# Optimization experiments

Hardware: AMD Instinct MI355X
Metric: run time of the kernel (lower is better)

Reference implementation:

```python
import jax, jax.numpy as jnp
import numpy as np

B, N, D, L, OUT = 4, 256, 256, 128, 256
GAMMA, ETA = 1e-4, 1.0


def _gcn_layer(x, alpha, adj, w_alpha, w_vi, w_vj, bias_h, w_node):
    # x:(B,N,D) alpha:(B,N,N,K) adj:(B,N,N)
    xi = jnp.einsum('bid,dk->bik', x, w_vi)  # project BEFORE broadcast (same math)
    xj = jnp.einsum('bjd,dk->bjk', x, w_vj)
    # bias_h:(D,K) broadcasts against trailing (N,K) dims (requires D==N, as in torch)
    H = jax.nn.relu(xi[:, :, None, :] + xj[:, None, :, :] + alpha + bias_h)  # (B,N,N,K)
    AH = jnp.einsum('bij,bijd->bid', adj, H)
    new_x = jax.nn.relu(jnp.einsum('bid,dk->bik', AH, w_node))
    new_alpha = jax.nn.relu(jnp.einsum('bijd,dk->bijk', H, w_alpha))
    return new_x, new_alpha


def setup_inputs() -> dict:
    key = jax.random.key(0)
    ks = jax.random.split(key, 20)
    inv = lambda fan: 1.0 / np.sqrt(fan)
    x = jax.random.normal(ks[0], (B, N, D), dtype=jnp.float32)
    rel_features = jax.random.normal(ks[1], (B, N, N, 6), dtype=jnp.float32)
    adj = jax.random.uniform(ks[2], (B, N, N), dtype=jnp.float32)
    box_num = jnp.concatenate(
        [jnp.full((1, 1), N, dtype=jnp.int32),
         jax.random.randint(ks[3], (B - 1, 1), N // 2, N + 1, dtype=jnp.int32)], axis=0)
    d = {
        'x': x, 'rel_features': rel_features, 'adj': adj, 'box_num': box_num,
        'W_alpha_t': jax.random.normal(ks[4], (6, D)) * inv(6),
        'b_alpha': jnp.zeros((D,), jnp.float32),
        'W_proj': jax.random.normal(ks[5], (D, L)) * inv(D),
        'b_proj': jnp.zeros((L,), jnp.float32),
        'learn_w': jax.random.uniform(ks[6], (L,)),
    }
    for li, base in ((0, 7), (1, 12)):
        d[f'l{li}_w_alpha'] = jax.random.normal(ks[base + 0], (D, OUT)) * inv(D)
        d[f'l{li}_w_vi'] = jax.random.normal(ks[base + 1], (D, OUT)) * inv(D)
        d[f'l{li}_w_vj'] = jax.random.normal(ks[base + 2], (D, OUT)) * inv(D)
        d[f'l{li}_bias_h'] = jax.random.uniform(ks[base + 3], (D, OUT))
        d[f'l{li}_w_node'] = jax.random.normal(ks[base + 4], (D, OUT)) * inv(D)
    return d


def reference(x, rel_features, adj, box_num, W_alpha_t, b_alpha, W_proj, b_proj, learn_w,
              l0_w_alpha, l0_w_vi, l0_w_vj, l0_bias_h, l0_w_node,
              l1_w_alpha, l1_w_vi, l1_w_vj, l1_bias_h, l1_w_node):
    alpha = jnp.einsum('bijc,cd->bijd', rel_features, W_alpha_t) + b_alpha  # (B,N,N,D)

    # ---- GraphLearningLayer ----
    x_hat = x @ W_proj + b_proj  # (B,N,L)
    valid = jnp.arange(N)[None, :] < box_num  # (B,N)
    pair = valid[:, None, :] & valid[:, :, None]  # (B,N,N)
    mask = jnp.where(pair, 0.0, -1.0)[..., None]  # (~mask)*-1 in torch
    dist = jnp.abs(x_hat[:, :, None, :] - x_hat[:, None, :, :]) + mask  # (B,N,N,L)
    out = jax.nn.leaky_relu(jnp.einsum('bijd,d->bij', dist, learn_w))
    out = out - jnp.max(out, axis=-1, keepdims=True)
    soft_adj = jnp.exp(out) * adj
    soft_adj = soft_adj / jnp.sum(soft_adj, axis=-1, keepdims=True) + 1e-10

    # graph learning loss (training branch)
    diff = x_hat[:, :, None, :] - x_hat[:, None, :, :]
    pair_norm = jnp.sqrt(jnp.sum(diff * diff, axis=-1) + 1e-12)  # (B,N,N)
    bn = box_num.astype(jnp.float32)[:, 0]
    dist_loss = jnp.sum(jnp.exp(soft_adj + ETA * pair_norm), axis=(1, 2)) / (bn * bn)
    f_norm = jnp.sqrt(jnp.sum(soft_adj * soft_adj, axis=(1, 2)))
    gl_loss = dist_loss + GAMMA * f_norm  # (B,)

    # ---- GCN stack ----
    adj2 = adj * soft_adj
    x1, alpha1 = _gcn_layer(x, alpha, adj2, l0_w_alpha, l0_w_vi, l0_w_vj, l0_bias_h, l0_w_node)
    x2, _ = _gcn_layer(x1, alpha1, adj2, l1_w_alpha, l1_w_vi, l1_w_vj, l1_bias_h, l1_w_node)
    return x2, soft_adj, gl_loss
```

## Files before the change

kernel.cpp:

```cpp
#include <hip/hip_runtime.h>
#include <hip/hip_bf16.h>

#define NB 4
#define NN 256
#define ND 256
#define NL 128
#define NK 256
static constexpr float GAMMA_C = 1e-4f;
static constexpr float ETA_C = 1.0f;

typedef unsigned int u32;
typedef __attribute__((ext_vector_type(8))) short bf16x8;
typedef __attribute__((ext_vector_type(4))) float f32x4;

__device__ __forceinline__ u32 rne1(float x) {
    u32 a = __float_as_uint(x);
    return (a + 0x7FFFu + ((a >> 16) & 1u)) >> 16;
}
__device__ __forceinline__ float bf2f(u32 v) { return __uint_as_float(v << 16); }
__device__ __forceinline__ u32 pk2(float lo, float hi) {
    union { __hip_bfloat162 h; u32 u; } cv;
    cv.h = __float22bfloat162_rn(make_float2(lo, hi));
    return cv.u;
}

struct GJob {
    const float* A; const float* W; const float* bias; const float* addm;
    float* C; float* CT; int Kd; int Nc; int relu;
};

__device__ __forceinline__ void gemm64_body(
    const float* __restrict__ A, const float* __restrict__ W,
    const float* __restrict__ bias, const float* __restrict__ addm,
    float* __restrict__ C, float* __restrict__ CT, int Kd, int Nc, int relu_act)
{
    __shared__ __align__(16) float As[16][68];
    __shared__ __align__(16) float Ws[16][64];
    int t = threadIdx.x;
    int r0 = blockIdx.x * 64, c0 = blockIdx.y * 64;
    int ty = t >> 4, tx = t & 15;
    float acc[4][4] = {};
    for (int kc = 0; kc < Kd; kc += 16) {
        __syncthreads();
        #pragma unroll
        for (int q = 0; q < 4; ++q) {
            int f = q * 256 + t;
            int row = f >> 4, kk = f & 15;
            As[kk][row] = A[(r0 + row) * Kd + kc + kk];
        }
        #pragma unroll
        for (int q = 0; q < 4; ++q) {
            int f = q * 256 + t;
            int kk = f >> 6, col = f & 63;
            Ws[kk][col] = W[(kc + kk) * Nc + c0 + col];
        }
        __syncthreads();
        #pragma unroll
        for (int kk = 0; kk < 16; ++kk) {
            float4 av = *(const float4*)&As[kk][ty * 4];
            float4 bv = *(const float4*)&Ws[kk][tx * 4];
            float a[4] = {av.x, av.y, av.z, av.w};
            float b[4] = {bv.x, bv.y, bv.z, bv.w};
            #pragma unroll
            for (int i = 0; i < 4; ++i)
                #pragma unroll
                for (int j = 0; j < 4; ++j)
                    acc[i][j] += a[i] * b[j];
        }
    }
    #pragma unroll
    for (int i = 0; i < 4; ++i) {
        int row = r0 + ty * 4 + i;
        #pragma unroll
        for (int j = 0; j < 4; ++j) {
            int col = c0 + tx * 4 + j;
            float v = acc[i][j];
            if (bias) v += bias[col];
            if (addm) v += addm[(row & 255) * Nc + col];
            if (relu_act) v = fmaxf(v, 0.f);
            C[row * Nc + col] = v;
            if (CT) CT[((row >> 8) * Nc + col) * 256 + (row & 255)] = v;
        }
    }
}

__global__ __launch_bounds__(256) void gemm64(
    const float* __restrict__ A, const float* __restrict__ W,
    const float* __restrict__ bias, const float* __restrict__ addm,
    float* __restrict__ C, int M, int Kd, int Nc, int relu_act)
{
    gemm64_body(A, W, bias, addm, C, nullptr, Kd, Nc, relu_act);
}

__global__ __launch_bounds__(256) void gemm64_multi(GJob j0, GJob j1, GJob j2)
{
    GJob jb = (blockIdx.z == 0) ? j0 : (blockIdx.z == 1) ? j1 : j2;
    if ((int)blockIdx.y * 64 >= jb.Nc) return;
    gemm64_body(jb.A, jb.W, jb.bias, jb.addm, jb.C, jb.CT, jb.Kd, jb.Nc, jb.relu);
}

__global__ __launch_bounds__(256) void soft_adj_kernel(
    const float* __restrict__ xhat, const float* __restrict__ xhatT,
    const float* __restrict__ adj,
    const int* __restrict__ box_num, const float* __restrict__ learn_w,
    float* __restrict__ soft_out, float* __restrict__ adj2,
    float* __restrict__ rowP1, float* __restrict__ rowP2)
{
    __shared__ __align__(16) float xs[NL];
    __shared__ __align__(16) float lw[NL];
    __shared__ float red[256];
    int bi = blockIdx.x;
    int b = bi >> 8, i = bi & 255;
    int j = threadIdx.x;
    if (j < NL) { xs[j] = xhat[bi * NL + j]; lw[j] = learn_w[j]; }
    __syncthreads();
    float sumw = 0.f;
    for (int d = 0; d < NL; ++d) sumw += lw[d];
    float s1 = 0.f, s2 = 0.f;
    const float* xT = &xhatT[(size_t)b * NL * 256];
    #pragma unroll 8
    for (int d = 0; d < NL; ++d) {
        float xjv = xT[d * 256 + j];
        float diff = xs[d] - xjv;
        s1 += fabsf(diff) * lw[d];
        s2 += diff * diff;
    }
    int bn = box_num[b];
    float maskv = (i < bn && j < bn) ? 0.f : -1.f;
    float out = s1 + maskv * sumw;
    out = (out >= 0.f) ? out : 0.01f * out;
    float pn = sqrtf(s2 + 1e-12f);
    red[j] = out; __syncthreads();
    for (int s = 128; s > 0; s >>= 1) { if (j < s) red[j] = fmaxf(red[j], red[j + s]); __syncthreads(); }
    float m = red[0]; __syncthreads();
    float aij = adj[bi * 256 + j];
    float e = expf(out - m) * aij;
    red[j] = e; __syncthreads();
    for (int s = 128; s > 0; s >>= 1) { if (j < s) red[j] += red[j + s]; __syncthreads(); }
    float S = red[0]; __syncthreads();
    float soft = e / S + 1e-10f;
    soft_out[bi * 256 + j] = soft;
    adj2[bi * 256 + j] = aij * soft;
    float p1 = expf(soft + ETA_C * pn);
    float p2 = soft * soft;
    red[j] = p1; __syncthreads();
    for (int s = 128; s > 0; s >>= 1) { if (j < s) red[j] += red[j + s]; __syncthreads(); }
    if (j == 0) rowP1[bi] = red[0];
    __syncthreads();
    red[j] = p2; __syncthreads();
    for (int s = 128; s > 0; s >>= 1) { if (j < s) red[j] += red[j + s]; __syncthreads(); }
    if (j == 0) rowP2[bi] = red[0];
}

__global__ __launch_bounds__(256) void gl_loss_kernel(
    const float* __restrict__ rowP1, const float* __restrict__ rowP2,
    const int* __restrict__ box_num, float* __restrict__ out)
{
    __shared__ float r1[256], r2[256];
    int b = blockIdx.x, t = threadIdx.x;
    r1[t] = rowP1[b * 256 + t];
    r2[t] = rowP2[b * 256 + t];
    __syncthreads();
    for (int s = 128; s > 0; s >>= 1) { if (t < s) { r1[t] += r1[t + s]; r2[t] += r2[t + s]; } __syncthreads(); }
    if (t == 0) {
        float bn = (float)box_num[b];
        out[b] = r1[0] / (bn * bn) + GAMMA_C * sqrtf(r2[0]);
    }
}

__global__ __launch_bounds__(256) void wprep(
    const float* __restrict__ w_alpha0, u32* __restrict__ wTp)
{
    int c = blockIdx.x >> 2, kgl = blockIdx.x & 3;
    int n = threadIdx.x;
    #pragma unroll
    for (int q = 0; q < 4; ++q) {
        int k = c * 32 + kgl * 8 + 2 * q;
        float w0 = w_alpha0[k * 256 + n];
        float w1 = w_alpha0[(k + 1) * 256 + n];
        u32 h0 = rne1(w0), h1 = rne1(w1);
        float l0 = w0 - bf2f(h0), l1 = w1 - bf2f(h1);
        wTp[(((0 * 8 + c) * 4 + kgl) * 256 + n) * 4 + q] = h0 | (h1 << 16);
        wTp[(((1 * 8 + c) * 4 + kgl) * 256 + n) * 4 + q] = rne1(l0) | (rne1(l1) << 16);
    }
}

__global__ __launch_bounds__(256, 3) void pass1M(
    const float* __restrict__ rel, const float* __restrict__ Wat,
    const float* __restrict__ b_alpha, const float* __restrict__ xi0,
    const float* __restrict__ xj0b, const float* __restrict__ adj2,
    const u32* __restrict__ wTp,
    u32* __restrict__ alpha1, float* __restrict__ ahpart)
{
    __shared__ __align__(16) float watb_s[256][8];
    __shared__ __align__(16) u32 hsA[2][4][64][4];
    __shared__ __align__(16) float st[16][260];

    int t = threadIdx.x;
    int jt = blockIdx.x, it = blockIdx.y, b = blockIdx.z;
    int i0 = it * 8, j0 = jt * 8;
    int m = t & 63, wv = t >> 6;
    int ii = m >> 3, jj = m & 7;
    int l4 = m >> 4, l16 = m & 15;

    #pragma unroll
    for (int q = 0; q < 8; ++q)
        watb_s[t][q] = (q < 6) ? Wat[q * 256 + t] : (q == 6 ? b_alpha[t] : 0.f);
    float relv2[6];
    #pragma unroll
    for (int c = 0; c < 6; ++c)
        relv2[c] = rel[((b * 256 + i0 + ii) * 256 + j0 + jj) * 6 + c];
    float adjv = adj2[(b * 256 + i0 + ii) * 256 + j0 + jj];
    float* ahbase = &ahpart[(((jt * 4 + b) * 32 + it) * 8 + ii) * 256];
    const float* xirow = &xi0[(b * 256 + i0 + ii) * 256];
    const float* xjrow = &xj0b[(b * 256 + j0 + jj) * 256];

    f32x4 acc[4][4];
    #pragma unroll
    for (int a = 0; a < 4; ++a)
        #pragma unroll
        for (int c = 0; c < 4; ++c)
            acc[a][c] = (f32x4){0.f, 0.f, 0.f, 0.f};

    __syncthreads();

    for (int c = 0; c < 8; ++c) {
        int db = c & 1;
        int kb = c * 32 + wv * 8;
        float xiarr[8], xjarr[8];
        {
            float4 x0 = *(const float4*)&xirow[kb];
            float4 x1 = *(const float4*)&xirow[kb + 4];
            xiarr[0]=x0.x; xiarr[1]=x0.y; xiarr[2]=x0.z; xiarr[3]=x0.w;
            xiarr[4]=x1.x; xiarr[5]=x1.y; xiarr[6]=x1.z; xiarr[7]=x1.w;
            float4 y0 = *(const float4*)&xjrow[kb];
            float4 y1 = *(const float4*)&xjrow[kb + 4];
            xjarr[0]=y0.x; xjarr[1]=y0.y; xjarr[2]=y0.z; xjarr[3]=y0.w;
            xjarr[4]=y1.x; xjarr[5]=y1.y; xjarr[6]=y1.z; xjarr[7]=y1.w;
        }
        float h[8];
        #pragma unroll
        for (int i = 0; i < 8; ++i) {
            int k = kb + i;
            float4 wa = *(const float4*)&watb_s[k][0];
            float4 wc = *(const float4*)&watb_s[k][4];
            float a = relv2[0]*wa.x + relv2[1]*wa.y + relv2[2]*wa.z + relv2[3]*wa.w
                    + relv2[4]*wc.x + relv2[5]*wc.y + wc.z;
            h[i] = fmaxf(xiarr[i] + xjarr[i] + a, 0.f);
        }
        {
            float ahv = 0.f;
            #pragma unroll
            for (int i = 0; i < 8; ++i) {
                float v = adjv * h[i];
                v += __shfl_xor(v, 1);
                v += __shfl_xor(v, 2);
                v += __shfl_xor(v, 4);
                ahv = (jj == i) ? v : ahv;
            }
            ahbase[kb + jj] = ahv;
        }
        {
            u32 hi[4];
            #pragma unroll
            for (int p = 0; p < 4; ++p)
                hi[p] = pk2(h[2*p], h[2*p+1]);
            *(uint4*)&hsA[db][wv][m][0] = make_uint4(hi[0], hi[1], hi[2], hi[3]);
        }
        __syncthreads();

        bf16x8 aH[4];
        #pragma unroll
        for (int mt = 0; mt < 4; ++mt)
            aH[mt] = *(const bf16x8*)&hsA[db][l4][mt * 16 + l16][0];
        const u32* wc0 = &wTp[(c * 4 + l4) * 1024];
        const u32* wc1 = &wTp[((8 + c) * 4 + l4) * 1024];
        #pragma unroll
        for (int ntl = 0; ntl < 4; ++ntl) {
            int n = (wv * 4 + ntl) * 16 + l16;
            bf16x8 bH = *(const bf16x8*)&wc0[n * 4];
            bf16x8 bL = *(const bf16x8*)&wc1[n * 4];
            #pragma unroll
            for (int mt = 0; mt < 4; ++mt) {
                acc[mt][ntl] = __builtin_amdgcn_mfma_f32_16x16x32_bf16(aH[mt], bH, acc[mt][ntl], 0, 0, 0);
                acc[mt][ntl] = __builtin_amdgcn_mfma_f32_16x16x32_bf16(aH[mt], bL, acc[mt][ntl], 0, 0, 0);
            }
        }
        __syncthreads();
    }

    #pragma unroll
    for (int mt = 0; mt < 4; ++mt) {
        #pragma unroll
        for (int ntl = 0; ntl < 4; ++ntl) {
            int n = (wv * 4 + ntl) * 16 + l16;
            #pragma unroll
            for (int r = 0; r < 4; ++r)
                st[l4 * 4 + r][n] = acc[mt][ntl][r];
        }
        __syncthreads();
        #pragma unroll
        for (int p = 0; p < 2; ++p) {
            int f = p * 256 + t;
            int row = f >> 5, u8 = f & 31;
            float4 c0 = *(const float4*)&st[row][u8 * 8];
            float4 c1 = *(const float4*)&st[row][u8 * 8 + 4];
            uint4 pk;
            pk.x = pk2(fmaxf(c0.x, 0.f), fmaxf(c0.y, 0.f));
            pk.y = pk2(fmaxf(c0.z, 0.f), fmaxf(c0.w, 0.f));
            pk.z = pk2(fmaxf(c1.x, 0.f), fmaxf(c1.y, 0.f));
            pk.w = pk2(fmaxf(c1.z, 0.f), fmaxf(c1.w, 0.f));
            int mg = mt * 16 + row;
            int iw = mg >> 3, jw = mg & 7;
            *(uint4*)&alpha1[((b * 256 + i0 + iw) * 256 + j0 + jw) * 128 + u8 * 4] = pk;
        }
        __syncthreads();
    }
}

__global__ __launch_bounds__(256) void post0(
    const float* __restrict__ part, const float* __restrict__ w_node0,
    const float* __restrict__ w_vi1, const float* __restrict__ w_vj1,
    const float* __restrict__ bias_h1,
    float* __restrict__ xi1, float* __restrict__ xj1b)
{
    __shared__ __align__(16) float ah_s[256];
    __shared__ __align__(16) float x1_s[256];
    int bi = blockIdx.x;
    int b = bi >> 8, i = bi & 255;
    int it = i >> 3, ii = i & 7;
    int t = threadIdx.x;
    float s = 0.f;
    #pragma unroll 4
    for (int jt = 0; jt < 32; ++jt)
        s += part[(((jt * 4 + b) * 32 + it) * 8 + ii) * 256 + t];
    ah_s[t] = s;
    __syncthreads();
    float a0 = 0.f;
    #pragma unroll 8
    for (int k = 0; k < 256; ++k)
        a0 += ah_s[k] * w_node0[k * 256 + t];
    x1_s[t] = fmaxf(a0, 0.f);
    __syncthreads();
    float a1 = 0.f, a2 = 0.f;
    #pragma unroll 8
    for (int k = 0; k < 256; ++k) {
        float xv = x1_s[k];
        a1 += xv * w_vi1[k * 256 + t];
        a2 += xv * w_vj1[k * 256 + t];
    }
    xi1[bi * 256 + t] = a1;
    xj1b[bi * 256 + t] = a2 + bias_h1[i * 256 + t];
}

__global__ __launch_bounds__(256) void pass2x(
    const u32* __restrict__ alpha1, const float* __restrict__ xi1,
    const float* __restrict__ xj1b, const float* __restrict__ adj2,
    const float* __restrict__ w_node1, float* __restrict__ x2)
{
    __shared__ __align__(16) float partial[4][256];
    __shared__ __align__(16) float ah1_s[256];
    int bi = blockIdx.x;
    int b = bi >> 8;
    int t = threadIdx.x;
    int wv = t >> 6, lane = t & 63;
    int k4 = lane * 4;
    float4 xi = *(const float4*)&xi1[bi * 256 + k4];
    float4 acc = {0.f, 0.f, 0.f, 0.f};
    size_t base = (size_t)bi * 32768;
    const float* a2row = &adj2[bi * 256];
    for (int j = wv; j < 256; j += 4) {
        float a2 = a2row[j];
        float4 xj = *(const float4*)&xj1b[(b * 256 + j) * 256 + k4];
        uint2 q = *(const uint2*)&alpha1[base + j * 128 + (k4 >> 1)];
        float4 al;
        al.x = bf2f(q.x & 0xFFFFu); al.y = bf2f(q.x >> 16);
        al.z = bf2f(q.y & 0xFFFFu); al.w = bf2f(q.y >> 16);
        acc.x += a2 * fmaxf(xi.x + xj.x + al.x, 0.f);
        acc.y += a2 * fmaxf(xi.y + xj.y + al.y, 0.f);
        acc.z += a2 * fmaxf(xi.z + xj.z + al.z, 0.f);
        acc.w += a2 * fmaxf(xi.w + xj.w + al.w, 0.f);
    }
    *(float4*)&partial[wv][k4] = acc;
    __syncthreads();
    ah1_s[t] = partial[0][t] + partial[1][t] + partial[2][t] + partial[3][t];
    __syncthreads();
    float a0 = 0.f;
    #pragma unroll 8
    for (int k = 0; k < 256; ++k)
        a0 += ah1_s[k] * w_node1[k * 256 + t];
    x2[bi * 256 + t] = fmaxf(a0, 0.f);
}

__global__ __launch_bounds__(256) void pass1C(
    const float* __restrict__ rel, const float* __restrict__ Wat,
    const float* __restrict__ b_alpha, const float* __restrict__ xi0,
    const float* __restrict__ xj0b, const float* __restrict__ adj2,
    float* __restrict__ AH0)
{
    __shared__ float xj_s[16][257];
    __shared__ float rel_s[16 * 48];
    __shared__ float adj_sC[128];
    int t = threadIdx.x;
    int it = blockIdx.x, b = blockIdx.y;
    int i0 = it * 8;
    float xiv[8], watv[6];
    #pragma unroll
    for (int ii = 0; ii < 8; ++ii) xiv[ii] = xi0[(b * 256 + i0 + ii) * 256 + t];
    #pragma unroll
    for (int c = 0; c < 6; ++c) watv[c] = Wat[c * 256 + t];
    float bav = b_alpha[t];
    float ah[8] = {};
    for (int jc = 0; jc < 256; jc += 16) {
        __syncthreads();
        #pragma unroll
        for (int q = 0; q < 16; ++q) xj_s[q][t] = xj0b[(b * 256 + jc + q) * 256 + t];
        for (int e = t; e < 768; e += 256) {
            int jjp = e / 48, r = e % 48;
            rel_s[e] = rel[((b * 256 + i0 + r / 6) * 256 + jc + jjp) * 6 + (r % 6)];
        }
        if (t < 128) adj_sC[t] = adj2[(b * 256 + i0 + (t & 7)) * 256 + jc + (t >> 3)];
        __syncthreads();
        for (int jjp = 0; jjp < 16; ++jjp) {
            float xjv = xj_s[jjp][t];
            #pragma unroll
            for (int ii = 0; ii < 8; ++ii) {
                float a = bav;
                #pragma unroll
                for (int c = 0; c < 6; ++c) a += rel_s[jjp * 48 + ii * 6 + c] * watv[c];
                float h = fmaxf(xiv[ii] + xjv + a, 0.f);
                ah[ii] += adj_sC[jjp * 8 + ii] * h;
            }
        }
    }
    #pragma unroll
    for (int ii = 0; ii < 8; ++ii)
        AH0[(b * 256 + i0 + ii) * 256 + t] = ah[ii];
}

__global__ __launch_bounds__(256) void pass2C(
    const float* __restrict__ rel, const float* __restrict__ Wat,
    const float* __restrict__ b_alpha, const float* __restrict__ xi0,
    const float* __restrict__ xj0b, const float* __restrict__ w_alpha0,
    const float* __restrict__ xi1, const float* __restrict__ xj1b,
    const float* __restrict__ adj2, float* __restrict__ AH1)
{
    __shared__ float xi_s[8][257];
    __shared__ float xj_s[8][257];
    __shared__ float xj1_s[8][257];
    __shared__ __align__(16) float wat_s[6][256];
    __shared__ __align__(16) float ba_s[256];
    __shared__ __align__(16) float rel_s[6][64];
    __shared__ __align__(16) float adj_s[64];
    __shared__ __align__(16) float hs[16][64];
    __shared__ __align__(16) float ws_s[16][256];

    int t = threadIdx.x;
    int it = blockIdx.x, b = blockIdx.y;
    int i0 = it * 8;
    int rg = t >> 5, cg = t & 31;
    int lane = t & 63, wv = t >> 6;
    int ii_l = lane >> 3, jj_l = lane & 7;

    #pragma unroll
    for (int q = 0; q < 8; ++q) xi_s[q][t] = xi0[(b * 256 + i0 + q) * 256 + t];
    #pragma unroll
    for (int q = 0; q < 6; ++q) wat_s[q][t] = Wat[q * 256 + t];
    ba_s[t] = b_alpha[t];
    float xi1v[8];
    #pragma unroll
    for (int y = 0; y < 8; ++y) xi1v[y] = xi1[(b * 256 + i0 + rg) * 256 + cg * 8 + y];
    float ah1[8] = {};

    for (int jt = 0; jt < 32; ++jt) {
        int j0 = jt * 8;
        __syncthreads();
        #pragma unroll
        for (int q = 0; q < 8; ++q) {
            xj_s[q][t]  = xj0b[(b * 256 + j0 + q) * 256 + t];
            xj1_s[q][t] = xj1b[(b * 256 + j0 + q) * 256 + t];
        }
        for (int e = t; e < 384; e += 256) {
            int ii = e / 48, rem = e % 48;
            int jjp = rem / 6, c = rem % 6;
            rel_s[c][ii * 8 + jjp] = rel[((b * 256 + i0 + ii) * 256 + j0 + jjp) * 6 + c];
        }
        if (t < 64) adj_s[t] = adj2[(b * 256 + i0 + (t >> 3)) * 256 + j0 + (t & 7)];

        float acc[8][8] = {};
        for (int c = 0; c < 16; ++c) {
            __syncthreads();
            #pragma unroll
            for (int p = 0; p < 4; ++p) {
                int klocal = wv + p * 4;
                int kg = c * 16 + klocal;
                float a = ba_s[kg];
                #pragma unroll
                for (int cc = 0; cc < 6; ++cc) a += rel_s[cc][lane] * wat_s[cc][kg];
                float h = xi_s[ii_l][kg] + xj_s[jj_l][kg] + a;
                hs[klocal][lane] = fmaxf(h, 0.f);
            }
            #pragma unroll
            for (int q = 0; q < 4; ++q) {
                int f = q * 256 + t;
                int row = f >> 6, col4 = f & 63;
                *(float4*)&ws_s[row][col4 * 4] =
                    *(const float4*)&w_alpha0[(c * 16 + row) * 256 + col4 * 4];
            }
            __syncthreads();
            #pragma unroll
            for (int kk = 0; kk < 16; ++kk) {
                float4 a0 = *(const float4*)&hs[kk][rg * 8];
                float4 a1 = *(const float4*)&hs[kk][rg * 8 + 4];
                float4 b0 = *(const float4*)&ws_s[kk][cg * 8];
                float4 b1 = *(const float4*)&ws_s[kk][cg * 8 + 4];
                float av[8] = {a0.x, a0.y, a0.z, a0.w, a1.x, a1.y, a1.z, a1.w};
                float bv[8] = {b0.x, b0.y, b0.z, b0.w, b1.x, b1.y, b1.z, b1.w};
                #pragma unroll
                for (int x = 0; x < 8; ++x)
                    #pragma unroll
                    for (int y = 0; y < 8; ++y)
                        acc[x][y] += av[x] * bv[y];
            }
        }
        #pragma unroll
        for (int x = 0; x < 8; ++x) {
            float a2 = adj_s[rg * 8 + x];
            #pragma unroll
            for (int y = 0; y < 8; ++y) {
                float al = fmaxf(acc[x][y], 0.f);
                float h1 = fmaxf(xi1v[y] + xj1_s[x][cg * 8 + y] + al, 0.f);
                ah1[y] += a2 * h1;
            }
        }
    }
    #pragma unroll
    for (int y = 0; y < 8; ++y)
        AH1[(b * 256 + i0 + rg) * 256 + cg * 8 + y] = ah1[y];
}

extern "C" void kernel_launch(void* const* d_in, const int* in_sizes, int n_in,
                              void* d_out, int out_size, void* d_ws, size_t ws_size,
                              hipStream_t stream)
{
    const float* x        = (const float*)d_in[0];
    const float* rel      = (const float*)d_in[1];
    const float* adj      = (const float*)d_in[2];
    const int*   box_num  = (const int*)d_in[3];
    const float* Wat      = (const float*)d_in[4];
    const float* b_alpha  = (const float*)d_in[5];
    const float* W_proj   = (const float*)d_in[6];
    const float* b_proj   = (const float*)d_in[7];
    const float* learn_w  = (const float*)d_in[8];
    const float* w_alpha0 = (const float*)d_in[9];
    const float* w_vi0    = (const float*)d_in[10];
    const float* w_vj0    = (const float*)d_in[11];
    const float* bias_h0  = (const float*)d_in[12];
    const float* w_node0  = (const float*)d_in[13];
    const float* w_vi1    = (const float*)d_in[15];
    const float* w_vj1    = (const float*)d_in[16];
    const float* bias_h1  = (const float*)d_in[17];
    const float* w_node1  = (const float*)d_in[18];

    float* sm    = (float*)d_ws;
    float* adj2  = sm;
    float* xhat  = adj2  + 262144;
    float* xi0   = xhat  + 131072;
    float* xj0b  = xi0   + 262144;
    float* AH0   = xj0b  + 262144;
    float* x1    = AH0   + 262144;
    float* xi1   = x1    + 262144;
    float* xj1b  = xi1   + 262144;
    float* AH1   = xj1b  + 262144;
    float* rowP1 = AH1   + 262144;
    float* rowP2 = rowP1 + 1024;
    float* xhatT = AH0;
    const size_t SMALLS_F = 2230272;
    const size_t WTP_F    = 65536;
    const size_t PART_F   = 8388608;
    u32*   wTp    = (u32*)(sm + SMALLS_F);
    float* part   = sm + SMALLS_F + WTP_F;
    u32*   alpha1 = (u32*)(sm + SMALLS_F + WTP_F + PART_F);

    const size_t needM = (SMALLS_F + WTP_F + PART_F) * 4ULL + 134217728ULL;
    int use_mfma = (ws_size >= needM);

    float* out_x2   = (float*)d_out;
    float* out_soft = out_x2 + 262144;
    float* out_gl   = out_soft + 262144;

    if (use_mfma) wprep<<<32, 256, 0, stream>>>(w_alpha0, wTp);

    {
        GJob ja{x, W_proj, b_proj, nullptr, xhat, xhatT, 256, 128, 0};
        GJob jb{x, w_vi0,  nullptr, nullptr, xi0,  nullptr, 256, 256, 0};
        GJob jc{x, w_vj0,  nullptr, bias_h0, xj0b, nullptr, 256, 256, 0};
        gemm64_multi<<<dim3(16, 4, 3), 256, 0, stream>>>(ja, jb, jc);
    }
    soft_adj_kernel<<<1024, 256, 0, stream>>>(xhat, xhatT, adj, box_num, learn_w, out_soft, adj2, rowP1, rowP2);
    gl_loss_kernel<<<4, 256, 0, stream>>>(rowP1, rowP2, box_num, out_gl);

    if (use_mfma) {
        pass1M<<<dim3(32, 32, 4), 256, 0, stream>>>(rel, Wat, b_alpha, xi0, xj0b, adj2, wTp, alpha1, part);
        post0<<<1024, 256, 0, stream>>>(part, w_node0, w_vi1, w_vj1, bias_h1, xi1, xj1b);
        pass2x<<<1024, 256, 0, stream>>>(alpha1, xi1, xj1b, adj2, w_node1, out_x2);
    } else {
        pass1C<<<dim3(32, 4), 256, 0, stream>>>(rel, Wat, b_alpha, xi0, xj0b, adj2, AH0);
        gemm64<<<dim3(16, 4), 256, 0, stream>>>(AH0, w_node0, nullptr, nullptr, x1, 1024, 256, 256, 1);
        {
            GJob j1a{x1, w_vi1, nullptr, nullptr, xi1,  nullptr, 256, 256, 0};
            GJob j1b{x1, w_vj1, nullptr, bias_h1, xj1b, nullptr, 256, 256, 0};
            gemm64_multi<<<dim3(16, 4, 2), 256, 0, stream>>>(j1a, j1b, j1b);
        }
        pass2C<<<dim3(32, 4), 256, 0, stream>>>(rel, Wat, b_alpha, xi0, xj0b, w_alpha0, xi1, xj1b, adj2, AH1);
        gemm64<<<dim3(16, 4), 256, 0, stream>>>(AH1, w_node1, nullptr, nullptr, out_x2, 1024, 256, 256, 1);
    }
}
```

Baseline: 417.8 us.

## Batch rows in post0/pass2x, prefetch xi/xj and drop a barrier in pass1M

post0 now handles four rows per block and pass2x two rows per block. This lets each loaded w_node0, w_vi1, w_vj1, w_node1 and xj1b value be reused across rows instead of reloaded per row. pass1M software-prefetches the next chunk's xi/xj vectors into registers, drops the trailing per-iteration __syncthreads (relying on the double-buffered hsA), and raises its occupancy hint from 3 to 4 waves per SIMD. The costs are higher register pressure, which may cause spills under the tighter launch bound, and fewer blocks in the post kernels, which reduces parallelism.

```diff
diff --git a/kernel.cpp b/kernel.cpp
--- a/kernel.cpp
+++ b/kernel.cpp
@@ -185,7 +185,7 @@
     }
 }
 
-__global__ __launch_bounds__(256, 3) void pass1M(
+__global__ __launch_bounds__(256, 4) void pass1M(
     const float* __restrict__ rel, const float* __restrict__ Wat,
     const float* __restrict__ b_alpha, const float* __restrict__ xi0,
     const float* __restrict__ xj0b, const float* __restrict__ adj2,
@@ -222,21 +222,27 @@
         for (int c = 0; c < 4; ++c)
             acc[a][c] = (f32x4){0.f, 0.f, 0.f, 0.f};
 
+    float4 pxi0 = *(const float4*)&xirow[wv * 8];
+    float4 pxi1 = *(const float4*)&xirow[wv * 8 + 4];
+    float4 pxj0 = *(const float4*)&xjrow[wv * 8];
+    float4 pxj1 = *(const float4*)&xjrow[wv * 8 + 4];
+
     __syncthreads();
 
     for (int c = 0; c < 8; ++c) {
         int db = c & 1;
         int kb = c * 32 + wv * 8;
         float xiarr[8], xjarr[8];
-        {
-            float4 x0 = *(const float4*)&xirow[kb];
-            float4 x1 = *(const float4*)&xirow[kb + 4];
-            xiarr[0]=x0.x; xiarr[1]=x0.y; xiarr[2]=x0.z; xiarr[3]=x0.w;
-            xiarr[4]=x1.x; xiarr[5]=x1.y; xiarr[6]=x1.z; xiarr[7]=x1.w;
-            float4 y0 = *(const float4*)&xjrow[kb];
-            float4 y1 = *(const float4*)&xjrow[kb + 4];
-            xjarr[0]=y0.x; xjarr[1]=y0.y; xjarr[2]=y0.z; xjarr[3]=y0.w;
-            xjarr[4]=y1.x; xjarr[5]=y1.y; xjarr[6]=y1.z; xjarr[7]=y1.w;
+        xiarr[0]=pxi0.x; xiarr[1]=pxi0.y; xiarr[2]=pxi0.z; xiarr[3]=pxi0.w;
+        xiarr[4]=pxi1.x; xiarr[5]=pxi1.y; xiarr[6]=pxi1.z; xiarr[7]=pxi1.w;
+        xjarr[0]=pxj0.x; xjarr[1]=pxj0.y; xjarr[2]=pxj0.z; xjarr[3]=pxj0.w;
+        xjarr[4]=pxj1.x; xjarr[5]=pxj1.y; xjarr[6]=pxj1.z; xjarr[7]=pxj1.w;
+        if (c < 7) {
+            int kn = kb + 32;
+            pxi0 = *(const float4*)&xirow[kn];
+            pxi1 = *(const float4*)&xirow[kn + 4];
+            pxj0 = *(const float4*)&xjrow[kn];
+            pxj1 = *(const float4*)&xjrow[kn + 4];
         }
         float h[8];
         #pragma unroll
@@ -286,7 +292,6 @@
                 acc[mt][ntl] = __builtin_amdgcn_mfma_f32_16x16x32_bf16(aH[mt], bL, acc[mt][ntl], 0, 0, 0);
             }
         }
-        __syncthreads();
     }
 
     #pragma unroll
@@ -324,33 +329,50 @@
     const float* __restrict__ bias_h1,
     float* __restrict__ xi1, float* __restrict__ xj1b)
 {
-    __shared__ __align__(16) float ah_s[256];
-    __shared__ __align__(16) float x1_s[256];
-    int bi = blockIdx.x;
-    int b = bi >> 8, i = bi & 255;
-    int it = i >> 3, ii = i & 7;
+    __shared__ __align__(16) float ah_s[4][256];
+    __shared__ __align__(16) float x1_s[4][256];
+    int bi0 = blockIdx.x * 4;
+    int b = bi0 >> 8;
     int t = threadIdx.x;
-    float s = 0.f;
-    #pragma unroll 4
-    for (int jt = 0; jt < 32; ++jt)
-        s += part[(((jt * 4 + b) * 32 + it) * 8 + ii) * 256 + t];
-    ah_s[t] = s;
-    __syncthreads();
-    float a0 = 0.f;
-    #pragma unroll 8
-    for (int k = 0; k < 256; ++k)
-        a0 += ah_s[k] * w_node0[k * 256 + t];
-    x1_s[t] = fmaxf(a0, 0.f);
-    __syncthreads();
-    float a1 = 0.f, a2 = 0.f;
+    #pragma unroll
+    for (int r = 0; r < 4; ++r) {
+        int i = (bi0 + r) & 255;
+        int it = i >> 3, ii = i & 7;
+        float s = 0.f;
+        #pragma unroll 4
+        for (int jt = 0; jt < 32; ++jt)
+            s += part[(((jt * 4 + b) * 32 + it) * 8 + ii) * 256 + t];
+        ah_s[r][t] = s;
+    }
+    __syncthreads();
+    float a0[4] = {};
     #pragma unroll 8
     for (int k = 0; k < 256; ++k) {
-        float xv = x1_s[k];
-        a1 += xv * w_vi1[k * 256 + t];
-        a2 += xv * w_vj1[k * 256 + t];
-    }
-    xi1[bi * 256 + t] = a1;
-    xj1b[bi * 256 + t] = a2 + bias_h1[i * 256 + t];
+        float w0 = w_node0[k * 256 + t];
+        #pragma unroll
+        for (int r = 0; r < 4; ++r) a0[r] += ah_s[r][k] * w0;
+    }
+    #pragma unroll
+    for (int r = 0; r < 4; ++r) x1_s[r][t] = fmaxf(a0[r], 0.f);
+    __syncthreads();
+    float a1[4] = {}, a2[4] = {};
+    #pragma unroll 8
+    for (int k = 0; k < 256; ++k) {
+        float w1 = w_vi1[k * 256 + t];
+        float w2 = w_vj1[k * 256 + t];
+        #pragma unroll
+        for (int r = 0; r < 4; ++r) {
+            float xv = x1_s[r][k];
+            a1[r] += xv * w1;
+            a2[r] += xv * w2;
+        }
+    }
+    #pragma unroll
+    for (int r = 0; r < 4; ++r) {
+        int i = (bi0 + r) & 255;
+        xi1[(bi0 + r) * 256 + t] = a1[r];
+        xj1b[(bi0 + r) * 256 + t] = a2[r] + bias_h1[i * 256 + t];
+    }
 }
 
 __global__ __launch_bounds__(256) void pass2x(
@@ -358,38 +380,55 @@
     const float* __restrict__ xj1b, const float* __restrict__ adj2,
     const float* __restrict__ w_node1, float* __restrict__ x2)
 {
-    __shared__ __align__(16) float partial[4][256];
-    __shared__ __align__(16) float ah1_s[256];
-    int bi = blockIdx.x;
-    int b = bi >> 8;
+    __shared__ __align__(16) float partial[4][2][256];
+    __shared__ __align__(16) float ah1_s[2][256];
+    int bi0 = blockIdx.x * 2;
+    int b = bi0 >> 8;
     int t = threadIdx.x;
     int wv = t >> 6, lane = t & 63;
     int k4 = lane * 4;
-    float4 xi = *(const float4*)&xi1[bi * 256 + k4];
-    float4 acc = {0.f, 0.f, 0.f, 0.f};
-    size_t base = (size_t)bi * 32768;
-    const float* a2row = &adj2[bi * 256];
+    float4 xiA = *(const float4*)&xi1[bi0 * 256 + k4];
+    float4 xiB = *(const float4*)&xi1[(bi0 + 1) * 256 + k4];
+    float4 accA = {0.f, 0.f, 0.f, 0.f};
+    float4 accB = {0.f, 0.f, 0.f, 0.f};
+    size_t baseA = (size_t)bi0 * 32768;
+    size_t baseB = baseA + 32768;
+    const float* a2A = &adj2[bi0 * 256];
+    const float* a2B = a2A + 256;
     for (int j = wv; j < 256; j += 4) {
-        float a2 = a2row[j];
         float4 xj = *(const float4*)&xj1b[(b * 256 + j) * 256 + k4];
-        uint2 q = *(const uint2*)&alpha1[base + j * 128 + (k4 >> 1)];
-        float4 al;
-        al.x = bf2f(q.x & 0xFFFFu); al.y = bf2f(q.x >> 16);
-        al.z = bf2f(q.y & 0xFFFFu); al.w = bf2f(q.y >> 16);
-        acc.x += a2 * fmaxf(xi.x + xj.x + al.x, 0.f);
-        acc.y += a2 * fmaxf(xi.y + xj.y + al.y, 0.f);
-        acc.z += a2 * fmaxf(xi.z + xj.z + al.z, 0.f);
-        acc.w += a2 * fmaxf(xi.w + xj.w + al.w, 0.f);
-    }
-    *(float4*)&partial[wv][k4] = acc;
-    __syncthreads();
-    ah1_s[t] = partial[0][t] + partial[1][t] + partial[2][t] + partial[3][t];
-    __syncthreads();
-    float a0 = 0.f;
+        float aA = a2A[j], aB = a2B[j];
+        uint2 qA = *(const uint2*)&alpha1[baseA + j * 128 + (k4 >> 1)];
+        uint2 qB = *(const uint2*)&alpha1[baseB + j * 128 + (k4 >> 1)];
+        float4 alA, alB;
+        alA.x = bf2f(qA.x & 0xFFFFu); alA.y = bf2f(qA.x >> 16);
+        alA.z = bf2f(qA.y & 0xFFFFu); alA.w = bf2f(qA.y >> 16);
+        alB.x = bf2f(qB.x & 0xFFFFu); alB.y = bf2f(qB.x >> 16);
+        alB.z = bf2f(qB.y & 0xFFFFu); alB.w = bf2f(qB.y >> 16);
+        accA.x += aA * fmaxf(xiA.x + xj.x + alA.x, 0.f);
+        accA.y += aA * fmaxf(xiA.y + xj.y + alA.y, 0.f);
+        accA.z += aA * fmaxf(xiA.z + xj.z + alA.z, 0.f);
+        accA.w += aA * fmaxf(xiA.w + xj.w + alA.w, 0.f);
+        accB.x += aB * fmaxf(xiB.x + xj.x + alB.x, 0.f);
+        accB.y += aB * fmaxf(xiB.y + xj.y + alB.y, 0.f);
+        accB.z += aB * fmaxf(xiB.z + xj.z + alB.z, 0.f);
+        accB.w += aB * fmaxf(xiB.w + xj.w + alB.w, 0.f);
+    }
+    *(float4*)&partial[wv][0][k4] = accA;
+    *(float4*)&partial[wv][1][k4] = accB;
+    __syncthreads();
+    ah1_s[0][t] = partial[0][0][t] + partial[1][0][t] + partial[2][0][t] + partial[3][0][t];
+    ah1_s[1][t] = partial[0][1][t] + partial[1][1][t] + partial[2][1][t] + partial[3][1][t];
+    __syncthreads();
+    float o0 = 0.f, o1 = 0.f;
     #pragma unroll 8
-    for (int k = 0; k < 256; ++k)
-        a0 += ah1_s[k] * w_node1[k * 256 + t];
-    x2[bi * 256 + t] = fmaxf(a0, 0.f);
+    for (int k = 0; k < 256; ++k) {
+        float w = w_node1[k * 256 + t];
+        o0 += ah1_s[0][k] * w;
+        o1 += ah1_s[1][k] * w;
+    }
+    x2[bi0 * 256 + t] = fmaxf(o0, 0.f);
+    x2[(bi0 + 1) * 256 + t] = fmaxf(o1, 0.f);
 }
 
 __global__ __launch_bounds__(256) void pass1C(
@@ -602,8 +641,8 @@
 
     if (use_mfma) {
         pass1M<<<dim3(32, 32, 4), 256, 0, stream>>>(rel, Wat, b_alpha, xi0, xj0b, adj2, wTp, alpha1, part);
-        post0<<<1024, 256, 0, stream>>>(part, w_node0, w_vi1, w_vj1, bias_h1, xi1, xj1b);
-        pass2x<<<1024, 256, 0, stream>>>(alpha1, xi1, xj1b, adj2, w_node1, out_x2);
+        post0<<<256, 256, 0, stream>>>(part, w_node0, w_vi1, w_vj1, bias_h1, xi1, xj1b);
+        pass2x<<<512, 256, 0, stream>>>(alpha1, xi1, xj1b, adj2, w_node1, out_x2);
     } else {
         pass1C<<<dim3(32, 4), 256, 0, stream>>>(rel, Wat, b_alpha, xi0, xj0b, adj2, AH0);
         gemm64<<<dim3(16, 4), 256, 0, stream>>>(AH0, w_node0, nullptr, nullptr, x1, 1024, 256, 256, 1);
```

After: 458.6 us. 9.8% more time.
